# Kernel tuning notes

Hardware: AMD Instinct MI355X
Metric: run time of the kernel (lower is better)

## Reference

```python
import jax, jax.numpy as jnp
from jax import lax
import numpy as np

B, T, K, H, D, KS = 4, 1024, 128, 8, 4, 5  # batch, seq, channels, heads, depth, kernel
EPS = 1e-5


def setup_inputs() -> dict:
    key = jax.random.key(0)
    ks = jax.random.split(key, 20)
    p = lambda i, shape: jax.random.normal(ks[i], shape, jnp.float32) * 0.02
    return {
        "x": jax.random.normal(ks[0], (B, T, K), jnp.float32),
        "pos_table": p(1, (T, K)),
        "q_w": p(2, (D, K * H, K, KS)), "q_b": p(3, (D, K * H)),
        "k_w": p(4, (D, K * H, K, KS)), "k_b": p(5, (D, K * H)),
        "v_w": p(6, (D, K * H, K, 1)),
        "uni_w": p(7, (D, K, K * H)), "uni_b": p(8, (D, K)),
        "ln1_s": jnp.ones((D, K), jnp.float32), "ln1_b": jnp.zeros((D, K), jnp.float32),
        "ln2_s": jnp.ones((D, K), jnp.float32), "ln2_b": jnp.zeros((D, K), jnp.float32),
        "ff1_w": p(9, (D, 4 * K, K)), "ff1_b": p(10, (D, 4 * K)),
        "ff2_w": p(11, (D, K, 4 * K)), "ff2_b": p(12, (D, K)),
        "mu_w": p(13, (1, K)), "mu_b": p(14, (1,)),
        "sig_w": p(15, (1, K)), "sig_b": p(16, (1,)),
    }


def _layernorm(x, s, b):
    m = jnp.mean(x, axis=-1, keepdims=True)
    v = jnp.mean((x - m) ** 2, axis=-1, keepdims=True)
    return (x - m) / jnp.sqrt(v + EPS) * s + b


def _causal_conv(x_nct, w, b):
    # x_nct: (b, k, t); w: (k*h, k, KS); left-pad for causal conv
    xp = jnp.pad(x_nct, ((0, 0), (0, 0), (KS - 1, 0)))
    y = lax.conv_general_dilated(xp, w, (1,), 'VALID',
                                 dimension_numbers=('NCH', 'OIH', 'NCH'))
    return y + b[None, :, None]


def _attention(x, qw, qb, kw, kb, vw, uw, ub):
    b, t, k = x.shape
    h = H
    xn = jnp.transpose(x, (0, 2, 1))  # (b, k, t)
    q = _causal_conv(xn, qw, qb)      # (b, k*h, t)
    ke = _causal_conv(xn, kw, kb)
    v = jnp.einsum('oi,bit->bot', vw[:, :, 0], xn)  # kernel-1 conv

    def prep(z, scale):
        z = z.reshape(b, k, h, t)
        z = jnp.transpose(z, (0, 2, 3, 1)) * scale        # (b, h, t, k)
        # faithful to torch: (b,h,t,k) -> transpose(1,2) -> (b,t,h,k) -> view(b*h,t,k)
        return jnp.transpose(z, (0, 2, 1, 3)).reshape(b * h, t, k)

    scale = k ** -0.25
    q, ke, v = prep(q, scale), prep(ke, scale), prep(v, 1.0)
    w = jnp.einsum('btk,bsk->bts', q, ke)              # (b*h, t, t)
    mask = jnp.triu(jnp.ones((t, t), bool), 1)
    w = jnp.where(mask[None], -jnp.inf, w)
    w = jax.nn.softmax(w, axis=2)
    o = jnp.einsum('bts,bsk->btk', w, v)
    o = o.reshape(b, h, t, k).transpose(0, 2, 1, 3).reshape(b, t, h * k)
    return o @ uw.T + ub


def _forward(x, pos_table, q_w, q_b, k_w, k_b, v_w, uni_w, uni_b,
             ln1_s, ln1_b, ln2_s, ln2_b, ff1_w, ff1_b, ff2_w, ff2_b,
             mu_w, mu_b, sig_w, sig_b):
    x = x + pos_table[None]
    for d in range(D):
        a = _attention(x, q_w[d], q_b[d], k_w[d], k_b[d], v_w[d], uni_w[d], uni_b[d])
        x = _layernorm(a + x, ln1_s[d], ln1_b[d])
        ff = jax.nn.relu(x @ ff1_w[d].T + ff1_b[d]) @ ff2_w[d].T + ff2_b[d]
        x = _layernorm(ff + x, ln2_s[d], ln2_b[d])
    mu = x @ mu_w.T + mu_b
    sigma = jax.nn.softplus(x @ sig_w.T + sig_b)
    return (mu, sigma)


def reference(x, pos_table, q_w, q_b, k_w, k_b, v_w, uni_w, uni_b,
              ln1_s, ln1_b, ln2_s, ln2_b, ff1_w, ff1_b, ff2_w, ff2_b,
              mu_w, mu_b, sig_w, sig_b):
    return _forward(x, pos_table, q_w, q_b, k_w, k_b, v_w, uni_w, uni_b,
                    ln1_s, ln1_b, ln2_s, ln2_b, ff1_w, ff1_b, ff2_w, ff2_b,
                    mu_w, mu_b, sig_w, sig_b)
```

## Files before the change

kernel.cpp:

```cpp
#include <hip/hip_runtime.h>
#include <math.h>

#define Bz 4
#define Tz 1024
#define Kz 128
#define Hz 8
#define Dz 4
#define KSz 5
#define EPSz 1e-5f
#define SCALEf 0.2973017787506803f

__global__ __launch_bounds__(256) void k_add_pos(const float* __restrict__ x,
                                                 const float* __restrict__ pos,
                                                 float* __restrict__ xb) {
    int i = blockIdx.x * 256 + threadIdx.x;
    const int n4 = Bz * Tz * Kz / 4;
    if (i >= n4) return;
    float4 xv = reinterpret_cast<const float4*>(x)[i];
    int tk = i % (Tz * Kz / 4);
    float4 pv = reinterpret_cast<const float4*>(pos)[tk];
    xv.x += pv.x; xv.y += pv.y; xv.z += pv.z; xv.w += pv.w;
    reinterpret_cast<float4*>(xb)[i] = xv;
}

__global__ __launch_bounds__(256) void k_tp_conv_t(const float* __restrict__ w,
                                                   float* __restrict__ wt) {
    const int oc0 = blockIdx.x << 6;
    const int ic0 = blockIdx.y << 4;
    const int d   = blockIdx.z;
    __shared__ float tile[64][81];
    const float* wb = w + ((long)d * 1024 + oc0) * 640 + ic0 * 5;
    for (int i = threadIdx.x; i < 64 * 80; i += 256) {
        int oc_l = i / 80, idx = i % 80;
        tile[oc_l][idx] = wb[(long)oc_l * 640 + idx];
    }
    __syncthreads();
    float* wo = wt + (long)d * 5 * 128 * 1024 + oc0;
    for (int j = threadIdx.x; j < 80 * 64; j += 256) {
        int oc_l = j & 63, r = j >> 6;
        int ic_l = r / 5, s = r - ic_l * 5;
        wo[((long)s * 128 + ic0 + ic_l) * 1024 + oc_l] = tile[oc_l][r];
    }
}

__global__ __launch_bounds__(256) void k_tp_mat_t(const float* __restrict__ in,
                                                  float* __restrict__ out,
                                                  int N, int Kd) {
    const int n0 = blockIdx.x << 5;
    const int k0 = blockIdx.y << 5;
    const int d  = blockIdx.z;
    __shared__ float t[32][33];
    const float* ib = in + ((long)d * N + n0) * Kd + k0;
    for (int i = threadIdx.x; i < 1024; i += 256) {
        int n_l = i >> 5, k_l = i & 31;
        t[n_l][k_l] = ib[(long)n_l * Kd + k_l];
    }
    __syncthreads();
    float* ob = out + ((long)d * Kd + k0) * N + n0;
    for (int j = threadIdx.x; j < 1024; j += 256) {
        int k_l = j >> 5, n_l = j & 31;
        ob[(long)k_l * N + n_l] = t[n_l][k_l];
    }
}

__global__ __launch_bounds__(512) void k_conv_qkv(
    const float* __restrict__ xb, const float* __restrict__ qT,
    const float* __restrict__ kT, const float* __restrict__ vT,
    const float* __restrict__ qb, const float* __restrict__ kb,
    float* __restrict__ Qp, float* __restrict__ Kp, float* __restrict__ Vp,
    int d)
{
    const int which = blockIdx.z;
    const int b  = blockIdx.x >> 4;
    const int t0 = (blockIdx.x & 15) << 6;
    const int oc0 = blockIdx.y << 8;
    __shared__ float xs[68][Kz];
    for (int i = threadIdx.x; i < 68 * (Kz / 4); i += 512) {
        int row = i >> 5, c4 = i & 31;
        int t = t0 - 4 + row;
        float4 v = make_float4(0.f, 0.f, 0.f, 0.f);
        if (t >= 0)
            v = reinterpret_cast<const float4*>(xb + ((long)b * Tz + t) * Kz)[c4];
        reinterpret_cast<float4*>(&xs[row][0])[c4] = v;
    }
    __syncthreads();

    const int ocq = threadIdx.x & 63;
    const int tg  = threadIdx.x >> 6;
    const int oc  = oc0 + ocq * 4;

    float acc[8][4];
#pragma unroll
    for (int i = 0; i < 8; ++i)
#pragma unroll
        for (int j = 0; j < 4; ++j) acc[i][j] = 0.f;

    const float* wbase = (which == 0) ? qT + (long)d * KSz * Kz * 1024
                       : (which == 1) ? kT + (long)d * KSz * Kz * 1024
                                      : vT + (long)d * Kz * 1024;

    if (which == 2) {
        for (int icb = 0; icb < Kz; icb += 4) {
            float4 xr[8];
#pragma unroll
            for (int i = 0; i < 8; ++i)
                xr[i] = *reinterpret_cast<const float4*>(&xs[tg * 8 + 4 + i][icb]);
#pragma unroll
            for (int u = 0; u < 4; ++u) {
                float4 wv = *reinterpret_cast<const float4*>(wbase + (icb + u) * 1024 + oc);
#pragma unroll
                for (int i = 0; i < 8; ++i) {
                    float xv = (&xr[i].x)[u];
                    acc[i][0] = fmaf(xv, wv.x, acc[i][0]);
                    acc[i][1] = fmaf(xv, wv.y, acc[i][1]);
                    acc[i][2] = fmaf(xv, wv.z, acc[i][2]);
                    acc[i][3] = fmaf(xv, wv.w, acc[i][3]);
                }
            }
        }
    } else {
        for (int icb = 0; icb < Kz; icb += 4) {
            float4 xr[12];
#pragma unroll
            for (int r = 0; r < 12; ++r)
                xr[r] = *reinterpret_cast<const float4*>(&xs[tg * 8 + r][icb]);
#pragma unroll
            for (int s = 0; s < KSz; ++s) {
#pragma unroll
                for (int u = 0; u < 4; ++u) {
                    float4 wv = *reinterpret_cast<const float4*>(
                        wbase + ((long)s * Kz + icb + u) * 1024 + oc);
#pragma unroll
                    for (int i = 0; i < 8; ++i) {
                        float x1 = (&xr[i + s].x)[u];
                        acc[i][0] = fmaf(x1, wv.x, acc[i][0]);
                        acc[i][1] = fmaf(x1, wv.y, acc[i][1]);
                        acc[i][2] = fmaf(x1, wv.z, acc[i][2]);
                        acc[i][3] = fmaf(x1, wv.w, acc[i][3]);
                    }
                }
            }
        }
    }

    float bias[4] = {0.f, 0.f, 0.f, 0.f};
    float scale = 1.f;
    if (which == 0) {
#pragma unroll
        for (int j = 0; j < 4; ++j) bias[j] = qb[d * 1024 + oc + j];
        scale = SCALEf;
    } else if (which == 1) {
#pragma unroll
        for (int j = 0; j < 4; ++j) bias[j] = kb[d * 1024 + oc + j];
        scale = SCALEf;
    }
    float* outp = (which == 0) ? Qp : (which == 1) ? Kp : Vp;
#pragma unroll
    for (int i = 0; i < 8; ++i) {
        int t = t0 + tg * 8 + i;
        long rb = ((long)b * Tz + t) * Hz;
#pragma unroll
        for (int j = 0; j < 4; ++j) {
            int occ = oc + j;
            outp[(rb + (occ & 7)) * Kz + (occ >> 3)] = (acc[i][j] + bias[j]) * scale;
        }
    }
}

__global__ __launch_bounds__(256) void k_attn(
    const float* __restrict__ Qp, const float* __restrict__ Kp,
    const float* __restrict__ Vp, float* __restrict__ attb)
{
    const int seq = blockIdx.y;
    __shared__ float qs[32][132];
    __shared__ float ksm[32][132];
    __shared__ float vs[32][128];
    __shared__ float ps[32][32];

    const int tid = threadIdx.x;
    const int ty = tid >> 4;
    const int tx = tid & 15;
    const int r0 = ty * 2, r1 = ty * 2 + 1;
    const int bb = seq >> 3, hh = seq & 7;

    for (int pass = 0; pass < 2; ++pass) {
        const int qt = pass ? (31 - (int)blockIdx.x) : (int)blockIdx.x;

        __syncthreads();
        const float* qbase = Qp + ((long)seq * Tz + qt * 32) * Kz;
        for (int i = tid; i < 32 * 32; i += 256) {
            int r = i >> 5, c4 = i & 31;
            float4 v = reinterpret_cast<const float4*>(qbase + r * Kz)[c4];
            *reinterpret_cast<float4*>(&qs[r][c4 * 4]) = v;
        }
        __syncthreads();

        float m0 = -INFINITY, m1 = -INFINITY, l0 = 0.f, l1 = 0.f;
        float o0[8], o1[8];
#pragma unroll
        for (int j = 0; j < 8; ++j) { o0[j] = 0.f; o1[j] = 0.f; }

        for (int kt = 0; kt <= qt; ++kt) {
            const float* kb2 = Kp + ((long)seq * Tz + kt * 32) * Kz;
            const float* vb2 = Vp + ((long)seq * Tz + kt * 32) * Kz;
            for (int i = tid; i < 32 * 32; i += 256) {
                int r = i >> 5, c4 = i & 31;
                float4 kv = reinterpret_cast<const float4*>(kb2 + r * Kz)[c4];
                *reinterpret_cast<float4*>(&ksm[r][c4 * 4]) = kv;
                float4 vv = reinterpret_cast<const float4*>(vb2 + r * Kz)[c4];
                reinterpret_cast<float4*>(&vs[r][0])[c4] = vv;
            }
            __syncthreads();

            float s00 = 0.f, s01 = 0.f, s10 = 0.f, s11 = 0.f;
#pragma unroll 8
            for (int c = 0; c < Kz; c += 4) {
                float4 q0 = *reinterpret_cast<const float4*>(&qs[r0][c]);
                float4 q1 = *reinterpret_cast<const float4*>(&qs[r1][c]);
                float4 ka = *reinterpret_cast<const float4*>(&ksm[tx][c]);
                float4 kb = *reinterpret_cast<const float4*>(&ksm[tx + 16][c]);
                s00 = fmaf(q0.x, ka.x, s00); s00 = fmaf(q0.y, ka.y, s00);
                s00 = fmaf(q0.z, ka.z, s00); s00 = fmaf(q0.w, ka.w, s00);
                s01 = fmaf(q0.x, kb.x, s01); s01 = fmaf(q0.y, kb.y, s01);
                s01 = fmaf(q0.z, kb.z, s01); s01 = fmaf(q0.w, kb.w, s01);
                s10 = fmaf(q1.x, ka.x, s10); s10 = fmaf(q1.y, ka.y, s10);
                s10 = fmaf(q1.z, ka.z, s10); s10 = fmaf(q1.w, ka.w, s10);
                s11 = fmaf(q1.x, kb.x, s11); s11 = fmaf(q1.y, kb.y, s11);
                s11 = fmaf(q1.z, kb.z, s11); s11 = fmaf(q1.w, kb.w, s11);
            }
            const int tq0 = qt * 32 + r0;
            const int skA = kt * 32 + tx;
            const int skB = kt * 32 + tx + 16;
            if (skA > tq0    ) s00 = -INFINITY;
            if (skB > tq0    ) s01 = -INFINITY;
            if (skA > tq0 + 1) s10 = -INFINITY;
            if (skB > tq0 + 1) s11 = -INFINITY;

            float rm0 = fmaxf(s00, s01), rm1 = fmaxf(s10, s11);
#pragma unroll
            for (int off = 1; off < 16; off <<= 1) {
                rm0 = fmaxf(rm0, __shfl_xor(rm0, off));
                rm1 = fmaxf(rm1, __shfl_xor(rm1, off));
            }
            float nm0 = fmaxf(m0, rm0), nm1 = fmaxf(m1, rm1);
            float p00 = __expf(s00 - nm0), p01 = __expf(s01 - nm0);
            float p10 = __expf(s10 - nm1), p11 = __expf(s11 - nm1);
            float rs0 = p00 + p01, rs1 = p10 + p11;
#pragma unroll
            for (int off = 1; off < 16; off <<= 1) {
                rs0 += __shfl_xor(rs0, off);
                rs1 += __shfl_xor(rs1, off);
            }
            float f0 = __expf(m0 - nm0), f1 = __expf(m1 - nm1);
            l0 = l0 * f0 + rs0;
            l1 = l1 * f1 + rs1;
            m0 = nm0; m1 = nm1;
#pragma unroll
            for (int j = 0; j < 8; ++j) { o0[j] *= f0; o1[j] *= f1; }
            ps[r0][tx] = p00; ps[r0][tx + 16] = p01;
            ps[r1][tx] = p10; ps[r1][tx + 16] = p11;
            __syncthreads();
#pragma unroll
            for (int kb4 = 0; kb4 < 8; ++kb4) {
                float4 p0v = *reinterpret_cast<const float4*>(&ps[r0][kb4 * 4]);
                float4 p1v = *reinterpret_cast<const float4*>(&ps[r1][kb4 * 4]);
#pragma unroll
                for (int u = 0; u < 4; ++u) {
                    int kk = kb4 * 4 + u;
                    float p0 = (&p0v.x)[u], p1 = (&p1v.x)[u];
                    float4 va = *reinterpret_cast<const float4*>(&vs[kk][4 * tx]);
                    float4 vb = *reinterpret_cast<const float4*>(&vs[kk][64 + 4 * tx]);
                    o0[0] = fmaf(p0, va.x, o0[0]); o0[1] = fmaf(p0, va.y, o0[1]);
                    o0[2] = fmaf(p0, va.z, o0[2]); o0[3] = fmaf(p0, va.w, o0[3]);
                    o0[4] = fmaf(p0, vb.x, o0[4]); o0[5] = fmaf(p0, vb.y, o0[5]);
                    o0[6] = fmaf(p0, vb.z, o0[6]); o0[7] = fmaf(p0, vb.w, o0[7]);
                    o1[0] = fmaf(p1, va.x, o1[0]); o1[1] = fmaf(p1, va.y, o1[1]);
                    o1[2] = fmaf(p1, va.z, o1[2]); o1[3] = fmaf(p1, va.w, o1[3]);
                    o1[4] = fmaf(p1, vb.x, o1[4]); o1[5] = fmaf(p1, vb.y, o1[5]);
                    o1[6] = fmaf(p1, vb.z, o1[6]); o1[7] = fmaf(p1, vb.w, o1[7]);
                }
            }
            __syncthreads();
        }
        float inv0 = 1.f / l0, inv1 = 1.f / l1;
        {
            int tt = qt * 32 + r0;
            float* op = attb + ((long)bb * Tz + tt) * (Hz * Kz) + hh * Kz;
            float4 w0 = make_float4(o0[0] * inv0, o0[1] * inv0, o0[2] * inv0, o0[3] * inv0);
            float4 w1 = make_float4(o0[4] * inv0, o0[5] * inv0, o0[6] * inv0, o0[7] * inv0);
            *reinterpret_cast<float4*>(op + 4 * tx) = w0;
            *reinterpret_cast<float4*>(op + 64 + 4 * tx) = w1;
        }
        {
            int tt = qt * 32 + r1;
            float* op = attb + ((long)bb * Tz + tt) * (Hz * Kz) + hh * Kz;
            float4 w0 = make_float4(o1[0] * inv1, o1[1] * inv1, o1[2] * inv1, o1[3] * inv1);
            float4 w1 = make_float4(o1[4] * inv1, o1[5] * inv1, o1[6] * inv1, o1[7] * inv1);
            *reinterpret_cast<float4*>(op + 4 * tx) = w0;
            *reinterpret_cast<float4*>(op + 64 + 4 * tx) = w1;
        }
    }
}

__global__ __launch_bounds__(256) void k_gemm2(
    const float* __restrict__ A, const float* __restrict__ WT,
    const float* __restrict__ bias, float* __restrict__ C,
    int N, int Kd, int relu,
    const float* __restrict__ biasA, long slabA, int fuseA)
{
    __shared__ float as[32][132];
    __shared__ float wsh[32][132];
    const int tid = threadIdx.x;
    const int m0 = blockIdx.x << 7;
    const int n0 = blockIdx.y << 7;
    const int rg = tid >> 4;
    const int cg = tid & 15;

    float acc[8][8];
#pragma unroll
    for (int i = 0; i < 8; ++i)
#pragma unroll
        for (int j = 0; j < 8; ++j) acc[i][j] = 0.f;

    const int ks = Kd / gridDim.z;
    const int kbeg = blockIdx.z * ks;
    const int kend = kbeg + ks;

    for (int k0 = kbeg; k0 < kend; k0 += 32) {
#pragma unroll
        for (int c = 0; c < 4; ++c) {
            int m = c * 32 + (tid >> 3);
            int kq = (tid & 7) * 4;
            long idx = (long)(m0 + m) * Kd + k0 + kq;
            float4 v = *reinterpret_cast<const float4*>(A + idx);
            if (fuseA) {
                float4 v1 = *reinterpret_cast<const float4*>(A + idx + slabA);
                float4 bA = *reinterpret_cast<const float4*>(biasA + k0 + kq);
                v.x = fmaxf(v.x + v1.x + bA.x, 0.f);
                v.y = fmaxf(v.y + v1.y + bA.y, 0.f);
                v.z = fmaxf(v.z + v1.z + bA.z, 0.f);
                v.w = fmaxf(v.w + v1.w + bA.w, 0.f);
            }
            as[kq + 0][m] = v.x; as[kq + 1][m] = v.y;
            as[kq + 2][m] = v.z; as[kq + 3][m] = v.w;
        }
#pragma unroll
        for (int c = 0; c < 4; ++c) {
            int kk = c * 8 + (tid >> 5);
            int nq = (tid & 31) * 4;
            float4 w = *reinterpret_cast<const float4*>(WT + (long)(k0 + kk) * N + n0 + nq);
            *reinterpret_cast<float4*>(&wsh[kk][nq]) = w;
        }
        __syncthreads();
#pragma unroll 4
        for (int kk = 0; kk < 32; ++kk) {
            float4 a0 = *reinterpret_cast<const float4*>(&as[kk][rg * 8]);
            float4 a1 = *reinterpret_cast<const float4*>(&as[kk][rg * 8 + 4]);
            float4 w0 = *reinterpret_cast<const float4*>(&wsh[kk][cg * 8]);
            float4 w1 = *reinterpret_cast<const float4*>(&wsh[kk][cg * 8 + 4]);
            float ar[8] = {a0.x, a0.y, a0.z, a0.w, a1.x, a1.y, a1.z, a1.w};
            float wr[8] = {w0.x, w0.y, w0.z, w0.w, w1.x, w1.y, w1.z, w1.w};
#pragma unroll
            for (int i = 0; i < 8; ++i)
#pragma unroll
                for (int j = 0; j < 8; ++j)
                    acc[i][j] = fmaf(ar[i], wr[j], acc[i][j]);
        }
        __syncthreads();
    }

    if (gridDim.z == 1) {
        float4 bv0 = *reinterpret_cast<const float4*>(bias + n0 + cg * 8);
        float4 bv1 = *reinterpret_cast<const float4*>(bias + n0 + cg * 8 + 4);
        float br[8] = {bv0.x, bv0.y, bv0.z, bv0.w, bv1.x, bv1.y, bv1.z, bv1.w};
#pragma unroll
        for (int i = 0; i < 8; ++i) {
            float v[8];
#pragma unroll
            for (int j = 0; j < 8; ++j) {
                v[j] = acc[i][j] + br[j];
                if (relu) v[j] = fmaxf(v[j], 0.f);
            }
            float* cp = C + (long)(m0 + rg * 8 + i) * N + n0 + cg * 8;
            *reinterpret_cast<float4*>(cp)     = make_float4(v[0], v[1], v[2], v[3]);
            *reinterpret_cast<float4*>(cp + 4) = make_float4(v[4], v[5], v[6], v[7]);
        }
    } else {
        float* outp = C + (long)blockIdx.z * 4096 * N;
#pragma unroll
        for (int i = 0; i < 8; ++i) {
            float* cp = outp + (long)(m0 + rg * 8 + i) * N + n0 + cg * 8;
            *reinterpret_cast<float4*>(cp)     = make_float4(acc[i][0], acc[i][1], acc[i][2], acc[i][3]);
            *reinterpret_cast<float4*>(cp + 4) = make_float4(acc[i][4], acc[i][5], acc[i][6], acc[i][7]);
        }
    }
}

__global__ __launch_bounds__(256) void k_add_ln_r(
    const float* __restrict__ P, int S, const float* __restrict__ gb,
    float* __restrict__ x, const float* __restrict__ sc, const float* __restrict__ bsh,
    const float* __restrict__ muw, const float* __restrict__ mub,
    const float* __restrict__ sgw, const float* __restrict__ sgb,
    float* __restrict__ outp)
{
    const int wave = threadIdx.x >> 6, lane = threadIdx.x & 63;
    const long row = (long)blockIdx.x * 4 + wave;
    float v0 = 0.f, v1 = 0.f;
    for (int si = 0; si < S; ++si) {
        float2 p = reinterpret_cast<const float2*>(P + (long)si * 4096 * Kz + row * Kz)[lane];
        v0 += p.x; v1 += p.y;
    }
    float2 g = reinterpret_cast<const float2*>(gb)[lane];
    float* xr = x + row * Kz;
    float2 xv = reinterpret_cast<const float2*>(xr)[lane];
    v0 += g.x + xv.x; v1 += g.y + xv.y;
    float sum = v0 + v1;
#pragma unroll
    for (int off = 1; off < 64; off <<= 1) sum += __shfl_xor(sum, off);
    float mean = sum * (1.f / Kz);
    float d0 = v0 - mean, d1 = v1 - mean;
    float vv = d0 * d0 + d1 * d1;
#pragma unroll
    for (int off = 1; off < 64; off <<= 1) vv += __shfl_xor(vv, off);
    float rstd = rsqrtf(vv * (1.f / Kz) + EPSz);
    float2 sv = reinterpret_cast<const float2*>(sc)[lane];
    float2 bv = reinterpret_cast<const float2*>(bsh)[lane];
    float2 ov;
    ov.x = d0 * rstd * sv.x + bv.x;
    ov.y = d1 * rstd * sv.y + bv.y;
    reinterpret_cast<float2*>(xr)[lane] = ov;

    if (outp) {
        float2 mw = reinterpret_cast<const float2*>(muw)[lane];
        float2 sw = reinterpret_cast<const float2*>(sgw)[lane];
        float am  = ov.x * mw.x + ov.y * mw.y;
        float as2 = ov.x * sw.x + ov.y * sw.y;
#pragma unroll
        for (int off = 1; off < 64; off <<= 1) {
            am  += __shfl_xor(am, off);
            as2 += __shfl_xor(as2, off);
        }
        if (lane == 0) {
            outp[row] = am + mub[0];
            float z = as2 + sgb[0];
            outp[(long)Bz * Tz + row] = (z > 20.f) ? z : log1pf(expf(z));
        }
    }
}

extern "C" void kernel_launch(void* const* d_in, const int* in_sizes, int n_in,
                              void* d_out, int out_size, void* d_ws, size_t ws_size,
                              hipStream_t stream) {
    const float* x     = (const float*)d_in[0];
    const float* pos   = (const float*)d_in[1];
    const float* q_w   = (const float*)d_in[2];
    const float* q_b   = (const float*)d_in[3];
    const float* k_w   = (const float*)d_in[4];
    const float* k_b   = (const float*)d_in[5];
    const float* v_w   = (const float*)d_in[6];
    const float* uni_w = (const float*)d_in[7];
    const float* uni_b = (const float*)d_in[8];
    const float* ln1_s = (const float*)d_in[9];
    const float* ln1_b = (const float*)d_in[10];
    const float* ln2_s = (const float*)d_in[11];
    const float* ln2_b = (const float*)d_in[12];
    const float* ff1_w = (const float*)d_in[13];
    const float* ff1_b = (const float*)d_in[14];
    const float* ff2_w = (const float*)d_in[15];
    const float* ff2_b = (const float*)d_in[16];
    const float* mu_w  = (const float*)d_in[17];
    const float* mu_b  = (const float*)d_in[18];
    const float* sig_w = (const float*)d_in[19];
    const float* sig_b = (const float*)d_in[20];
    float* out = (float*)d_out;

    float* ws   = (float*)d_ws;
    float* xb   = ws;
    float* qT   = xb   + 524288;
    float* kT   = qT   + 2621440;
    float* vT   = kT   + 2621440;
    float* uniT = vT   + 524288;
    float* f1T  = uniT + 524288;
    float* f2T  = f1T  + 262144;
    float* Qp   = f2T  + 262144;
    float* Kp   = Qp   + 4194304;
    float* Vp   = Kp   + 4194304;
    float* attb = Vp   + 4194304;
    float* Pp   = attb + 4194304;

    k_add_pos<<<512, 256, 0, stream>>>(x, pos, xb);

    k_tp_conv_t<<<dim3(16, 8, Dz), 256, 0, stream>>>(q_w, qT);
    k_tp_conv_t<<<dim3(16, 8, Dz), 256, 0, stream>>>(k_w, kT);
    k_tp_mat_t<<<dim3(32, 4, Dz), 256, 0, stream>>>(v_w,   vT,   1024, 128);
    k_tp_mat_t<<<dim3(4, 32, Dz), 256, 0, stream>>>(uni_w, uniT, 128, 1024);
    k_tp_mat_t<<<dim3(16, 4, Dz), 256, 0, stream>>>(ff1_w, f1T,  512, 128);
    k_tp_mat_t<<<dim3(4, 16, Dz), 256, 0, stream>>>(ff2_w, f2T,  128, 512);

    for (int d = 0; d < Dz; ++d) {
        const int last = (d == Dz - 1);
        k_conv_qkv<<<dim3(64, 4, 3), 512, 0, stream>>>(
            xb, qT, kT, vT, q_b, k_b, Qp, Kp, Vp, d);
        k_attn<<<dim3(16, 32), 256, 0, stream>>>(Qp, Kp, Vp, attb);
        k_gemm2<<<dim3(32, 1, 8), 256, 0, stream>>>(
            attb, uniT + (long)d * 1024 * 128, uni_b + d * 128, Pp, 128, 1024, 0,
            nullptr, 0, 0);
        k_add_ln_r<<<1024, 256, 0, stream>>>(
            Pp, 8, uni_b + d * 128, xb, ln1_s + d * 128, ln1_b + d * 128,
            nullptr, nullptr, nullptr, nullptr, nullptr);
        k_gemm2<<<dim3(32, 4, 2), 256, 0, stream>>>(
            xb, f1T + (long)d * 128 * 512, ff1_b + d * 512, Pp, 512, 128, 1,
            nullptr, 0, 0);
        k_gemm2<<<dim3(32, 1, 8), 256, 0, stream>>>(
            Pp, f2T + (long)d * 512 * 128, ff2_b + d * 128, attb, 128, 512, 0,
            ff1_b + d * 512, (long)4096 * 512, 1);
        k_add_ln_r<<<1024, 256, 0, stream>>>(
            attb, 8, ff2_b + d * 128, xb, ln2_s + d * 128, ln2_b + d * 128,
            last ? mu_w : nullptr, last ? mu_b : nullptr,
            last ? sig_w : nullptr, last ? sig_b : nullptr,
            last ? out : nullptr);
    }
}
```

Measured before the change: 1.851 ms.

## Register-prefetch next K/V tile in attention and launch one query tile per block

The attention kernel now loads the next K/V tile into registers while computing on the current tile held in shared memory, so global load latency overlaps compute. The two-pass pairing of query tiles per block (for causal load balance) is dropped in favour of one query tile per block on a grid twice as wide. Launch bounds now request 3 blocks per SM. This trades in-block load balancing for more parallel blocks, and raises register pressure from the 8 float4 prefetch buffers.

Result: slower. 3.016 ms (+62.9%).

```diff
diff --git a/kernel.cpp b/kernel.cpp
--- a/kernel.cpp
+++ b/kernel.cpp
@@ -167,10 +167,11 @@
     }
 }
 
-__global__ __launch_bounds__(256) void k_attn(
+__global__ __launch_bounds__(256, 3) void k_attn(
     const float* __restrict__ Qp, const float* __restrict__ Kp,
     const float* __restrict__ Vp, float* __restrict__ attb)
 {
+    const int qt  = blockIdx.x;
     const int seq = blockIdx.y;
     __shared__ float qs[32][132];
     __shared__ float ksm[32][132];
@@ -182,123 +183,139 @@
     const int tx = tid & 15;
     const int r0 = ty * 2, r1 = ty * 2 + 1;
     const int bb = seq >> 3, hh = seq & 7;
-
-    for (int pass = 0; pass < 2; ++pass) {
-        const int qt = pass ? (31 - (int)blockIdx.x) : (int)blockIdx.x;
-
+    const int sr  = tid >> 5;
+    const int sc4 = tid & 31;
+
+    const float* qbase = Qp + ((long)seq * Tz + qt * 32) * Kz;
+    for (int i = tid; i < 32 * 32; i += 256) {
+        int r = i >> 5, c4 = i & 31;
+        float4 v = reinterpret_cast<const float4*>(qbase + r * Kz)[c4];
+        *reinterpret_cast<float4*>(&qs[r][c4 * 4]) = v;
+    }
+
+    float4 kpre[4], vpre[4];
+    {
+        const float* kb2 = Kp + (long)seq * Tz * Kz;
+        const float* vb2 = Vp + (long)seq * Tz * Kz;
+#pragma unroll
+        for (int it = 0; it < 4; ++it) {
+            int r = sr + it * 8;
+            kpre[it] = reinterpret_cast<const float4*>(kb2 + r * Kz)[sc4];
+            vpre[it] = reinterpret_cast<const float4*>(vb2 + r * Kz)[sc4];
+        }
+    }
+
+    float m0 = -INFINITY, m1 = -INFINITY, l0 = 0.f, l1 = 0.f;
+    float o0[8], o1[8];
+#pragma unroll
+    for (int j = 0; j < 8; ++j) { o0[j] = 0.f; o1[j] = 0.f; }
+
+    for (int kt = 0; kt <= qt; ++kt) {
+#pragma unroll
+        for (int it = 0; it < 4; ++it) {
+            int r = sr + it * 8;
+            *reinterpret_cast<float4*>(&ksm[r][sc4 * 4]) = kpre[it];
+            reinterpret_cast<float4*>(&vs[r][0])[sc4] = vpre[it];
+        }
         __syncthreads();
-        const float* qbase = Qp + ((long)seq * Tz + qt * 32) * Kz;
-        for (int i = tid; i < 32 * 32; i += 256) {
-            int r = i >> 5, c4 = i & 31;
-            float4 v = reinterpret_cast<const float4*>(qbase + r * Kz)[c4];
-            *reinterpret_cast<float4*>(&qs[r][c4 * 4]) = v;
-        }
+
+        if (kt < qt) {
+            const float* kb2 = Kp + ((long)seq * Tz + (kt + 1) * 32) * Kz;
+            const float* vb2 = Vp + ((long)seq * Tz + (kt + 1) * 32) * Kz;
+#pragma unroll
+            for (int it = 0; it < 4; ++it) {
+                int r = sr + it * 8;
+                kpre[it] = reinterpret_cast<const float4*>(kb2 + r * Kz)[sc4];
+                vpre[it] = reinterpret_cast<const float4*>(vb2 + r * Kz)[sc4];
+            }
+        }
+
+        float s00 = 0.f, s01 = 0.f, s10 = 0.f, s11 = 0.f;
+#pragma unroll 8
+        for (int c = 0; c < Kz; c += 4) {
+            float4 q0 = *reinterpret_cast<const float4*>(&qs[r0][c]);
+            float4 q1 = *reinterpret_cast<const float4*>(&qs[r1][c]);
+            float4 ka = *reinterpret_cast<const float4*>(&ksm[tx][c]);
+            float4 kb = *reinterpret_cast<const float4*>(&ksm[tx + 16][c]);
+            s00 = fmaf(q0.x, ka.x, s00); s00 = fmaf(q0.y, ka.y, s00);
+            s00 = fmaf(q0.z, ka.z, s00); s00 = fmaf(q0.w, ka.w, s00);
+            s01 = fmaf(q0.x, kb.x, s01); s01 = fmaf(q0.y, kb.y, s01);
+            s01 = fmaf(q0.z, kb.z, s01); s01 = fmaf(q0.w, kb.w, s01);
+            s10 = fmaf(q1.x, ka.x, s10); s10 = fmaf(q1.y, ka.y, s10);
+            s10 = fmaf(q1.z, ka.z, s10); s10 = fmaf(q1.w, ka.w, s10);
+            s11 = fmaf(q1.x, kb.x, s11); s11 = fmaf(q1.y, kb.y, s11);
+            s11 = fmaf(q1.z, kb.z, s11); s11 = fmaf(q1.w, kb.w, s11);
+        }
+        const int tq0 = qt * 32 + r0;
+        const int skA = kt * 32 + tx;
+        const int skB = kt * 32 + tx + 16;
+        if (skA > tq0    ) s00 = -INFINITY;
+        if (skB > tq0    ) s01 = -INFINITY;
+        if (skA > tq0 + 1) s10 = -INFINITY;
+        if (skB > tq0 + 1) s11 = -INFINITY;
+
+        float rm0 = fmaxf(s00, s01), rm1 = fmaxf(s10, s11);
+#pragma unroll
+        for (int off = 1; off < 16; off <<= 1) {
+            rm0 = fmaxf(rm0, __shfl_xor(rm0, off));
+            rm1 = fmaxf(rm1, __shfl_xor(rm1, off));
+        }
+        float nm0 = fmaxf(m0, rm0), nm1 = fmaxf(m1, rm1);
+        float p00 = __expf(s00 - nm0), p01 = __expf(s01 - nm0);
+        float p10 = __expf(s10 - nm1), p11 = __expf(s11 - nm1);
+        float rs0 = p00 + p01, rs1 = p10 + p11;
+#pragma unroll
+        for (int off = 1; off < 16; off <<= 1) {
+            rs0 += __shfl_xor(rs0, off);
+            rs1 += __shfl_xor(rs1, off);
+        }
+        float f0 = __expf(m0 - nm0), f1 = __expf(m1 - nm1);
+        l0 = l0 * f0 + rs0;
+        l1 = l1 * f1 + rs1;
+        m0 = nm0; m1 = nm1;
+#pragma unroll
+        for (int j = 0; j < 8; ++j) { o0[j] *= f0; o1[j] *= f1; }
+        ps[r0][tx] = p00; ps[r0][tx + 16] = p01;
+        ps[r1][tx] = p10; ps[r1][tx + 16] = p11;
         __syncthreads();
-
-        float m0 = -INFINITY, m1 = -INFINITY, l0 = 0.f, l1 = 0.f;
-        float o0[8], o1[8];
-#pragma unroll
-        for (int j = 0; j < 8; ++j) { o0[j] = 0.f; o1[j] = 0.f; }
-
-        for (int kt = 0; kt <= qt; ++kt) {
-            const float* kb2 = Kp + ((long)seq * Tz + kt * 32) * Kz;
-            const float* vb2 = Vp + ((long)seq * Tz + kt * 32) * Kz;
-            for (int i = tid; i < 32 * 32; i += 256) {
-                int r = i >> 5, c4 = i & 31;
-                float4 kv = reinterpret_cast<const float4*>(kb2 + r * Kz)[c4];
-                *reinterpret_cast<float4*>(&ksm[r][c4 * 4]) = kv;
-                float4 vv = reinterpret_cast<const float4*>(vb2 + r * Kz)[c4];
-                reinterpret_cast<float4*>(&vs[r][0])[c4] = vv;
+#pragma unroll
+        for (int kb4 = 0; kb4 < 8; ++kb4) {
+            float4 p0v = *reinterpret_cast<const float4*>(&ps[r0][kb4 * 4]);
+            float4 p1v = *reinterpret_cast<const float4*>(&ps[r1][kb4 * 4]);
+#pragma unroll
+            for (int u = 0; u < 4; ++u) {
+                int kk = kb4 * 4 + u;
+                float p0 = (&p0v.x)[u], p1 = (&p1v.x)[u];
+                float4 va = *reinterpret_cast<const float4*>(&vs[kk][4 * tx]);
+                float4 vb = *reinterpret_cast<const float4*>(&vs[kk][64 + 4 * tx]);
+                o0[0] = fmaf(p0, va.x, o0[0]); o0[1] = fmaf(p0, va.y, o0[1]);
+                o0[2] = fmaf(p0, va.z, o0[2]); o0[3] = fmaf(p0, va.w, o0[3]);
+                o0[4] = fmaf(p0, vb.x, o0[4]); o0[5] = fmaf(p0, vb.y, o0[5]);
+                o0[6] = fmaf(p0, vb.z, o0[6]); o0[7] = fmaf(p0, vb.w, o0[7]);
+                o1[0] = fmaf(p1, va.x, o1[0]); o1[1] = fmaf(p1, va.y, o1[1]);
+                o1[2] = fmaf(p1, va.z, o1[2]); o1[3] = fmaf(p1, va.w, o1[3]);
+                o1[4] = fmaf(p1, vb.x, o1[4]); o1[5] = fmaf(p1, vb.y, o1[5]);
+                o1[6] = fmaf(p1, vb.z, o1[6]); o1[7] = fmaf(p1, vb.w, o1[7]);
             }
-            __syncthreads();
-
-            float s00 = 0.f, s01 = 0.f, s10 = 0.f, s11 = 0.f;
-#pragma unroll 8
-            for (int c = 0; c < Kz; c += 4) {
-                float4 q0 = *reinterpret_cast<const float4*>(&qs[r0][c]);
-                float4 q1 = *reinterpret_cast<const float4*>(&qs[r1][c]);
-                float4 ka = *reinterpret_cast<const float4*>(&ksm[tx][c]);
-                float4 kb = *reinterpret_cast<const float4*>(&ksm[tx + 16][c]);
-                s00 = fmaf(q0.x, ka.x, s00); s00 = fmaf(q0.y, ka.y, s00);
-                s00 = fmaf(q0.z, ka.z, s00); s00 = fmaf(q0.w, ka.w, s00);
-                s01 = fmaf(q0.x, kb.x, s01); s01 = fmaf(q0.y, kb.y, s01);
-                s01 = fmaf(q0.z, kb.z, s01); s01 = fmaf(q0.w, kb.w, s01);
-                s10 = fmaf(q1.x, ka.x, s10); s10 = fmaf(q1.y, ka.y, s10);
-                s10 = fmaf(q1.z, ka.z, s10); s10 = fmaf(q1.w, ka.w, s10);
-                s11 = fmaf(q1.x, kb.x, s11); s11 = fmaf(q1.y, kb.y, s11);
-                s11 = fmaf(q1.z, kb.z, s11); s11 = fmaf(q1.w, kb.w, s11);
-            }
-            const int tq0 = qt * 32 + r0;
-            const int skA = kt * 32 + tx;
-            const int skB = kt * 32 + tx + 16;
-            if (skA > tq0    ) s00 = -INFINITY;
-            if (skB > tq0    ) s01 = -INFINITY;
-            if (skA > tq0 + 1) s10 = -INFINITY;
-            if (skB > tq0 + 1) s11 = -INFINITY;
-
-            float rm0 = fmaxf(s00, s01), rm1 = fmaxf(s10, s11);
-#pragma unroll
-            for (int off = 1; off < 16; off <<= 1) {
-                rm0 = fmaxf(rm0, __shfl_xor(rm0, off));
-                rm1 = fmaxf(rm1, __shfl_xor(rm1, off));
-            }
-            float nm0 = fmaxf(m0, rm0), nm1 = fmaxf(m1, rm1);
-            float p00 = __expf(s00 - nm0), p01 = __expf(s01 - nm0);
-            float p10 = __expf(s10 - nm1), p11 = __expf(s11 - nm1);
-            float rs0 = p00 + p01, rs1 = p10 + p11;
-#pragma unroll
-            for (int off = 1; off < 16; off <<= 1) {
-                rs0 += __shfl_xor(rs0, off);
-                rs1 += __shfl_xor(rs1, off);
-            }
-            float f0 = __expf(m0 - nm0), f1 = __expf(m1 - nm1);
-            l0 = l0 * f0 + rs0;
-            l1 = l1 * f1 + rs1;
-            m0 = nm0; m1 = nm1;
-#pragma unroll
-            for (int j = 0; j < 8; ++j) { o0[j] *= f0; o1[j] *= f1; }
-            ps[r0][tx] = p00; ps[r0][tx + 16] = p01;
-            ps[r1][tx] = p10; ps[r1][tx + 16] = p11;
-            __syncthreads();
-#pragma unroll
-            for (int kb4 = 0; kb4 < 8; ++kb4) {
-                float4 p0v = *reinterpret_cast<const float4*>(&ps[r0][kb4 * 4]);
-                float4 p1v = *reinterpret_cast<const float4*>(&ps[r1][kb4 * 4]);
-#pragma unroll
-                for (int u = 0; u < 4; ++u) {
-                    int kk = kb4 * 4 + u;
-                    float p0 = (&p0v.x)[u], p1 = (&p1v.x)[u];
-                    float4 va = *reinterpret_cast<const float4*>(&vs[kk][4 * tx]);
-                    float4 vb = *reinterpret_cast<const float4*>(&vs[kk][64 + 4 * tx]);
-                    o0[0] = fmaf(p0, va.x, o0[0]); o0[1] = fmaf(p0, va.y, o0[1]);
-                    o0[2] = fmaf(p0, va.z, o0[2]); o0[3] = fmaf(p0, va.w, o0[3]);
-                    o0[4] = fmaf(p0, vb.x, o0[4]); o0[5] = fmaf(p0, vb.y, o0[5]);
-                    o0[6] = fmaf(p0, vb.z, o0[6]); o0[7] = fmaf(p0, vb.w, o0[7]);
-                    o1[0] = fmaf(p1, va.x, o1[0]); o1[1] = fmaf(p1, va.y, o1[1]);
-                    o1[2] = fmaf(p1, va.z, o1[2]); o1[3] = fmaf(p1, va.w, o1[3]);
-                    o1[4] = fmaf(p1, vb.x, o1[4]); o1[5] = fmaf(p1, vb.y, o1[5]);
-                    o1[6] = fmaf(p1, vb.z, o1[6]); o1[7] = fmaf(p1, vb.w, o1[7]);
-                }
-            }
-            __syncthreads();
-        }
-        float inv0 = 1.f / l0, inv1 = 1.f / l1;
-        {
-            int tt = qt * 32 + r0;
-            float* op = attb + ((long)bb * Tz + tt) * (Hz * Kz) + hh * Kz;
-            float4 w0 = make_float4(o0[0] * inv0, o0[1] * inv0, o0[2] * inv0, o0[3] * inv0);
-            float4 w1 = make_float4(o0[4] * inv0, o0[5] * inv0, o0[6] * inv0, o0[7] * inv0);
-            *reinterpret_cast<float4*>(op + 4 * tx) = w0;
-            *reinterpret_cast<float4*>(op + 64 + 4 * tx) = w1;
-        }
-        {
-            int tt = qt * 32 + r1;
-            float* op = attb + ((long)bb * Tz + tt) * (Hz * Kz) + hh * Kz;
-            float4 w0 = make_float4(o1[0] * inv1, o1[1] * inv1, o1[2] * inv1, o1[3] * inv1);
-            float4 w1 = make_float4(o1[4] * inv1, o1[5] * inv1, o1[6] * inv1, o1[7] * inv1);
-            *reinterpret_cast<float4*>(op + 4 * tx) = w0;
-            *reinterpret_cast<float4*>(op + 64 + 4 * tx) = w1;
-        }
+        }
+        __syncthreads();
+    }
+    float inv0 = 1.f / l0, inv1 = 1.f / l1;
+    {
+        int tt = qt * 32 + r0;
+        float* op = attb + ((long)bb * Tz + tt) * (Hz * Kz) + hh * Kz;
+        float4 w0 = make_float4(o0[0] * inv0, o0[1] * inv0, o0[2] * inv0, o0[3] * inv0);
+        float4 w1 = make_float4(o0[4] * inv0, o0[5] * inv0, o0[6] * inv0, o0[7] * inv0);
+        *reinterpret_cast<float4*>(op + 4 * tx) = w0;
+        *reinterpret_cast<float4*>(op + 64 + 4 * tx) = w1;
+    }
+    {
+        int tt = qt * 32 + r1;
+        float* op = attb + ((long)bb * Tz + tt) * (Hz * Kz) + hh * Kz;
+        float4 w0 = make_float4(o1[0] * inv1, o1[1] * inv1, o1[2] * inv1, o1[3] * inv1);
+        float4 w1 = make_float4(o1[4] * inv1, o1[5] * inv1, o1[6] * inv1, o1[7] * inv1);
+        *reinterpret_cast<float4*>(op + 4 * tx) = w0;
+        *reinterpret_cast<float4*>(op + 64 + 4 * tx) = w1;
     }
 }
 
@@ -501,7 +518,7 @@
         const int last = (d == Dz - 1);
         k_conv_qkv<<<dim3(64, 4, 3), 512, 0, stream>>>(
             xb, qT, kT, vT, q_b, k_b, Qp, Kp, Vp, d);
-        k_attn<<<dim3(16, 32), 256, 0, stream>>>(Qp, Kp, Vp, attb);
+        k_attn<<<dim3(32, 32), 256, 0, stream>>>(Qp, Kp, Vp, attb);
         k_gemm2<<<dim3(32, 1, 8), 256, 0, stream>>>(
             attb, uniT + (long)d * 1024 * 128, uni_b + d * 128, Pp, 128, 1024, 0,
             nullptr, 0, 0);
```
